# Kernel optimization log

Measured on AMD Instinct MI355X. Metric: run time of the kernel, lower is better.

The kernel has to match this reference:

```python
import jax, jax.numpy as jnp
import numpy as np
import math

SL, BS, D, NH, PF, STRIDE, LAYERS = 2048, 4, 512, 8, 3, 1, 1
DH = D // NH
N_SPF = 9  # 0-2: hidden (a,t,v cross-attend to raw inputs); 3-5: cross (at,tv,va, shared for reverse dir); 6-8: self
EMBED_SCALE = math.sqrt(D)


def _ln(x, g, b):
    m = x.mean(-1, keepdims=True)
    var = ((x - m) ** 2).mean(-1, keepdims=True)
    return (x - m) / jnp.sqrt(var + 1e-5) * g + b


def _sinusoid(sl, d):
    half = d // 2
    inv = jnp.exp(jnp.arange(half, dtype=jnp.float32) * (-math.log(10000.0) / (half - 1)))
    ang = jnp.arange(sl, dtype=jnp.float32)[:, None] * inv[None, :]
    return jnp.concatenate([jnp.sin(ang), jnp.cos(ang)], axis=-1)  # (sl, d)


def setup_inputs() -> dict:
    key = jax.random.key(0)
    ks = jax.random.split(key, 16)
    s = 0.02
    p = {}
    p['a'] = jax.random.normal(ks[0], (SL, BS, D), jnp.float32)
    p['t'] = jax.random.normal(ks[1], (SL, BS, D), jnp.float32)
    p['v'] = jax.random.normal(ks[2], (SL, BS, D), jnp.float32)
    p['init_hiddens'] = s * jax.random.normal(ks[3], (3, D), jnp.float32)
    # stacked MultiheadAttention weights for the 9 SPF blocks
    p['wq'] = s * jax.random.normal(ks[4], (N_SPF, D, D), jnp.float32)
    p['bq'] = jnp.zeros((N_SPF, D), jnp.float32)
    p['wk'] = s * jax.random.normal(ks[5], (N_SPF, D, D), jnp.float32)
    p['bk'] = jnp.zeros((N_SPF, D), jnp.float32)
    p['wv'] = s * jax.random.normal(ks[6], (N_SPF, D, D), jnp.float32)
    p['bv'] = jnp.zeros((N_SPF, D), jnp.float32)
    p['wo'] = s * jax.random.normal(ks[7], (N_SPF, D, D), jnp.float32)
    p['bo'] = jnp.zeros((N_SPF, D), jnp.float32)
    p['ln_g'] = jnp.ones((N_SPF, D), jnp.float32)
    p['ln_b'] = jnp.zeros((N_SPF, D), jnp.float32)
    p['lnkv_g'] = jnp.ones((N_SPF, D), jnp.float32)
    p['lnkv_b'] = jnp.zeros((N_SPF, D), jnp.float32)
    # stacked FFN weights for the 9 FFN blocks
    p['w1'] = s * jax.random.normal(ks[8], (N_SPF, 4 * D, D), jnp.float32)
    p['b1'] = jnp.zeros((N_SPF, 4 * D), jnp.float32)
    p['w2'] = s * jax.random.normal(ks[9], (N_SPF, D, 4 * D), jnp.float32)
    p['b2'] = jnp.zeros((N_SPF, D), jnp.float32)
    p['fln_g'] = jnp.ones((N_SPF, D), jnp.float32)
    p['fln_b'] = jnp.zeros((N_SPF, D), jnp.float32)
    p['out_g'] = jnp.ones((D,), jnp.float32)
    p['out_b'] = jnp.zeros((D,), jnp.float32)
    return p


def reference(a, t, v, init_hiddens, wq, bq, wk, bk, wv, bv, wo, bo,
              ln_g, ln_b, lnkv_g, lnkv_b, w1, b1, w2, b2, fln_g, fln_b,
              out_g, out_b):
    scale = DH ** -0.5
    # precomputed strided modulo gather indices: r[i,j] = (i+1)*stride - pf + j
    idx = ((jnp.arange(SL) + 1) * STRIDE - PF)[:, None] + jnp.arange(PF)[None, :]  # (SL, PF)

    def spf(i, x, ctx, has_kv):
        # x: (SL, BS, D); ctx: (CL, BS, D) or None (self-attention on normed x)
        res = x
        xn = _ln(x, ln_g[i], ln_b[i])
        c = xn if ctx is None else ctx
        kv = c[idx % c.shape[0]]                      # (SL, PF, BS, D) modulo-gathered window
        if has_kv:
            kv = _ln(kv, lnkv_g[i], lnkv_b[i])
        q = (xn @ wq[i].T + bq[i]).reshape(SL, BS, NH, DH) * scale
        k = (kv @ wk[i].T + bk[i]).reshape(SL, PF, BS, NH, DH)
        vv = (kv @ wv[i].T + bv[i]).reshape(SL, PF, BS, NH, DH)
        attn = jax.nn.softmax(jnp.einsum('sbnd,spbnd->sbnp', q, k), axis=-1)
        o = jnp.einsum('sbnp,spbnd->sbnd', attn, vv).reshape(SL, BS, D)
        return res + o @ wo[i].T + bo[i]

    def ffn(i, x):
        h = jax.nn.relu(_ln(x, fln_g[i], fln_b[i]) @ w1[i].T + b1[i])
        return x + h @ w2[i].T + b2[i]

    pos = _sinusoid(SL, D)[:, None, :]
    a = a * EMBED_SCALE + pos
    t = t * EMBED_SCALE + pos
    v = v * EMBED_SCALE + pos
    h_a = jnp.broadcast_to(init_hiddens[0], (SL, BS, D))
    h_t = jnp.broadcast_to(init_hiddens[1], (SL, BS, D))
    h_v = jnp.broadcast_to(init_hiddens[2], (SL, BS, D))

    for _ in range(LAYERS):
        # hidden layer: hiddens cross-attend to raw modality streams
        h_a = ffn(0, spf(0, h_a, a, True))
        h_t = ffn(1, spf(1, h_t, t, True))
        h_v = ffn(2, spf(2, h_v, v, True))
        # cross layer: six branches, three shared weight sets (forward/reverse)
        h_at = ffn(3, spf(3, h_a, h_t, True))
        h_tv = ffn(4, spf(4, h_t, h_v, True))
        h_va = ffn(5, spf(5, h_v, h_a, True))
        h_ta = ffn(3, spf(3, h_t, h_a, True))
        h_vt = ffn(4, spf(4, h_v, h_t, True))
        h_av = ffn(5, spf(5, h_a, h_v, True))
        h_a, h_t, h_v = h_at + h_av, h_ta + h_tv, h_va + h_vt
        # self layer
        h_a = ffn(6, spf(6, h_a, None, False))
        h_t = ffn(7, spf(7, h_t, None, False))
        h_v = ffn(8, spf(8, h_v, None, False))

    return jnp.stack([_ln(h_a, out_g, out_b), _ln(h_t, out_g, out_b), _ln(h_v, out_g, out_b)])
```

## Files before the change

kernel.cpp:

```cpp
#include <hip/hip_runtime.h>

#define SL 2048
#define BS 4
#define DM 512
#define NH 8
#define DH 64
#define RD 8192
#define DF 2048

#define BM 128
#define BK 32

typedef unsigned short u16;
typedef __attribute__((ext_vector_type(8))) short short8;
typedef __attribute__((ext_vector_type(4))) float f32x4;

__device__ __forceinline__ float bf2f(u16 u) {
  return __uint_as_float(((unsigned)u) << 16);
}
__device__ __forceinline__ u16 f2bf(float f) {
  unsigned u = __float_as_uint(f);
  unsigned r = (u + 0x7fffu + ((u >> 16) & 1u)) >> 16;
  return (u16)r;
}

typedef __attribute__((address_space(3))) unsigned int lds_u32;
typedef __attribute__((address_space(1))) unsigned int gbl_u32;
__device__ __forceinline__ void gload_lds16(const void* g, void* l) {
  __builtin_amdgcn_global_load_lds((gbl_u32*)g, (lds_u32*)l, 16, 0, 0);
}

struct GemmDesc {
  const u16* A;
  const u16* B;
  const float* bias;
  const float* res;
  u16* Cb;
  float* Cf;
  float bmul;
  int relu;
  int accum;
};
struct GemmBatch { GemmDesc d[9]; };

struct LnDesc { const float* x; const float* g; const float* b; u16* yb; float* yf; };
struct LnBatch { LnDesc d[6]; };

struct AttnDesc { const u16* Q; const u16* K; const u16* V; u16* O; };
struct AttnBatch { AttnDesc d[3]; };

struct CvtDesc { const float* src; u16* dst; int n8; float scale; };
struct CvtBatch { CvtDesc d[6]; };

struct EmbBatch { const float* src[3]; float* dst[3]; const float* pos; };

template<int TBN>
__global__ __launch_bounds__(256) void gemm_k(GemmBatch args, int N, int K) {
  constexpr int NFR = TBN / 32;
  constexpr int BU = TBN / 64;
  GemmDesc g = args.d[blockIdx.z];
  __shared__ u16 As[2][BM * BK];
  __shared__ u16 Bs[2][TBN * BK];
  const int t = threadIdx.x;
  const int w = t >> 6, l = t & 63;
  const u16* Ag = g.A + (size_t)blockIdx.y * BM * K;
  const u16* Bg = g.B + (size_t)blockIdx.x * TBN * K;
  f32x4 acc[4][NFR];
#pragma unroll
  for (int m = 0; m < 4; ++m)
#pragma unroll
    for (int n = 0; n < NFR; ++n) acc[m][n] = f32x4{0.f, 0.f, 0.f, 0.f};
  const int wr = (w >> 1) * 64;
  const int wc = (w & 1) * (TBN / 2);
  const int lr = l & 15;
  const int cxo = ((l >> 4) ^ (l & 3)) << 3;

  auto stage = [&](int buf, int k0) {
#pragma unroll
    for (int i = 0; i < 2; ++i) {
      const int u = (i << 8) + t;
      const int row = u >> 2;
      const int c = (u & 3) ^ (row & 3);
      gload_lds16(Ag + (size_t)row * K + k0 + (c << 3),
                  (char*)&As[buf][0] + (i << 12) + (w << 10));
    }
#pragma unroll
    for (int i = 0; i < BU; ++i) {
      const int u = (i << 8) + t;
      const int row = u >> 2;
      const int c = (u & 3) ^ (row & 3);
      gload_lds16(Bg + (size_t)row * K + k0 + (c << 3),
                  (char*)&Bs[buf][0] + (i << 12) + (w << 10));
    }
  };

  stage(0, 0);
  const int nt = K / BK;
  int cur = 0;
  for (int it = 0; it < nt; ++it) {
    __syncthreads();
    if (it + 1 < nt) stage(cur ^ 1, (it + 1) * BK);
    const u16* Ab = &As[cur][0];
    const u16* Bb = &Bs[cur][0];
    short8 af[4], bfr[NFR];
#pragma unroll
    for (int m = 0; m < 4; ++m)
      af[m] = *(const short8*)(Ab + (wr + m * 16 + lr) * BK + cxo);
#pragma unroll
    for (int n = 0; n < NFR; ++n)
      bfr[n] = *(const short8*)(Bb + (wc + n * 16 + lr) * BK + cxo);
#pragma unroll
    for (int m = 0; m < 4; ++m)
#pragma unroll
      for (int n = 0; n < NFR; ++n)
        acc[m][n] = __builtin_amdgcn_mfma_f32_16x16x32_bf16(af[m], bfr[n], acc[m][n], 0, 0, 0);
    cur ^= 1;
  }

  const int c0 = blockIdx.x * TBN + wc + lr;
  const int r0 = blockIdx.y * BM + wr + ((l >> 4) << 2);
#pragma unroll
  for (int n = 0; n < NFR; ++n) {
    const int gc = c0 + n * 16;
    const float bi = g.bias ? g.bias[gc] * g.bmul : 0.f;
#pragma unroll
    for (int m = 0; m < 4; ++m) {
#pragma unroll
      for (int r = 0; r < 4; ++r) {
        const size_t off = (size_t)(r0 + m * 16 + r) * N + gc;
        float v = acc[m][n][r] + bi;
        if (g.res) v += g.res[off];
        if (g.relu) v = fmaxf(v, 0.f);
        if (g.Cb) {
          g.Cb[off] = f2bf(v);
        } else {
          if (g.accum) v += g.Cf[off];
          g.Cf[off] = v;
        }
      }
    }
  }
}

__global__ __launch_bounds__(256) void ln_k(LnBatch args) {
  LnDesc d = args.d[blockIdx.y];
  const int row = blockIdx.x * 4 + (threadIdx.x >> 6);
  const int l = threadIdx.x & 63;
  const float* xp = d.x + (size_t)row * DM + l * 8;
  float4 x0 = *(const float4*)xp;
  float4 x1 = *(const float4*)(xp + 4);
  float xv[8] = {x0.x, x0.y, x0.z, x0.w, x1.x, x1.y, x1.z, x1.w};
  float s = 0.f, ss = 0.f;
#pragma unroll
  for (int j = 0; j < 8; ++j) { s += xv[j]; ss += xv[j] * xv[j]; }
#pragma unroll
  for (int m = 1; m < 64; m <<= 1) {
    s += __shfl_xor(s, m, 64);
    ss += __shfl_xor(ss, m, 64);
  }
  const float mean = s * (1.f / DM);
  const float var = ss * (1.f / DM) - mean * mean;
  const float rstd = rsqrtf(var + 1e-5f);
  float4 g0 = *(const float4*)(d.g + l * 8);
  float4 g1 = *(const float4*)(d.g + l * 8 + 4);
  float4 b0 = *(const float4*)(d.b + l * 8);
  float4 b1 = *(const float4*)(d.b + l * 8 + 4);
  float gv[8] = {g0.x, g0.y, g0.z, g0.w, g1.x, g1.y, g1.z, g1.w};
  float bv[8] = {b0.x, b0.y, b0.z, b0.w, b1.x, b1.y, b1.z, b1.w};
  float y[8];
#pragma unroll
  for (int j = 0; j < 8; ++j) y[j] = (xv[j] - mean) * rstd * gv[j] + bv[j];
  if (d.yb) {
    short8 p;
#pragma unroll
    for (int j = 0; j < 8; ++j) p[j] = (short)f2bf(y[j]);
    *(short8*)(d.yb + (size_t)row * DM + l * 8) = p;
  } else {
    float* o = d.yf + (size_t)row * DM + l * 8;
    *(float4*)o = float4{y[0], y[1], y[2], y[3]};
    *(float4*)(o + 4) = float4{y[4], y[5], y[6], y[7]};
  }
}

__global__ __launch_bounds__(256) void attn_k(AttnBatch args) {
  AttnDesc d = args.d[blockIdx.y];
  const int idx = blockIdx.x * 256 + threadIdx.x;
  const int h = idx & 7;
  const int b = (idx >> 3) & 3;
  const int s = idx >> 5;
  const int s0 = (s + SL - 2) & (SL - 1);
  const int s1 = (s + SL - 1) & (SL - 1);
  const size_t rq = (size_t)(s * BS + b) * DM + h * DH;
  const size_t r0 = (size_t)(s0 * BS + b) * DM + h * DH;
  const size_t r1 = (size_t)(s1 * BS + b) * DM + h * DH;
  float d0 = 0.f, d1 = 0.f, d2 = 0.f;
#pragma unroll
  for (int c = 0; c < 8; ++c) {
    short8 q8 = *(const short8*)(d.Q + rq + c * 8);
    short8 k0 = *(const short8*)(d.K + r0 + c * 8);
    short8 k1 = *(const short8*)(d.K + r1 + c * 8);
    short8 k2 = *(const short8*)(d.K + rq + c * 8);
#pragma unroll
    for (int e = 0; e < 8; ++e) {
      const float q = bf2f((u16)q8[e]);
      d0 += q * bf2f((u16)k0[e]);
      d1 += q * bf2f((u16)k1[e]);
      d2 += q * bf2f((u16)k2[e]);
    }
  }
  const float mx = fmaxf(d0, fmaxf(d1, d2));
  float e0 = expf(d0 - mx), e1 = expf(d1 - mx), e2 = expf(d2 - mx);
  const float inv = 1.f / (e0 + e1 + e2);
  e0 *= inv; e1 *= inv; e2 *= inv;
#pragma unroll
  for (int c = 0; c < 8; ++c) {
    short8 v0 = *(const short8*)(d.V + r0 + c * 8);
    short8 v1 = *(const short8*)(d.V + r1 + c * 8);
    short8 v2 = *(const short8*)(d.V + rq + c * 8);
    short8 o8;
#pragma unroll
    for (int e = 0; e < 8; ++e)
      o8[e] = (short)f2bf(e0 * bf2f((u16)v0[e]) + e1 * bf2f((u16)v1[e]) + e2 * bf2f((u16)v2[e]));
    *(short8*)(d.O + rq + c * 8) = o8;
  }
}

__global__ __launch_bounds__(256) void cvt_k(CvtBatch a) {
  CvtDesc d = a.d[blockIdx.y];
  const int stride = gridDim.x * 256;
  for (int i = blockIdx.x * 256 + threadIdx.x; i < d.n8; i += stride) {
    float4 x0 = ((const float4*)d.src)[i * 2];
    float4 x1 = ((const float4*)d.src)[i * 2 + 1];
    short8 r;
    r[0] = (short)f2bf(x0.x * d.scale); r[1] = (short)f2bf(x0.y * d.scale);
    r[2] = (short)f2bf(x0.z * d.scale); r[3] = (short)f2bf(x0.w * d.scale);
    r[4] = (short)f2bf(x1.x * d.scale); r[5] = (short)f2bf(x1.y * d.scale);
    r[6] = (short)f2bf(x1.z * d.scale); r[7] = (short)f2bf(x1.w * d.scale);
    *(short8*)(d.dst + (size_t)i * 8) = r;
  }
}

__global__ __launch_bounds__(256) void pos_k(float* pos) {
  const int i = blockIdx.x * 256 + threadIdx.x;
  const int dd = i & (DM - 1);
  const int s = i >> 9;
  const int j = (dd < 256) ? dd : dd - 256;
  const float inv = expf((float)j * -0.036119374f);
  const float ang = (float)s * inv;
  pos[i] = (dd < 256) ? sinf(ang) : cosf(ang);
}

__global__ __launch_bounds__(256) void embed_k(EmbBatch a) {
  const int z = blockIdx.y;
  const int i = blockIdx.x * 256 + threadIdx.x;
  float4 x = ((const float4*)a.src[z])[i];
  const int e = i << 2;
  const int dcol = e & (DM - 1);
  const int srow = e >> 11;
  float4 p = *(const float4*)(a.pos + (size_t)srow * DM + dcol);
  const float SC = 22.627417f;
  float4 y{x.x * SC + p.x, x.y * SC + p.y, x.z * SC + p.z, x.w * SC + p.w};
  ((float4*)a.dst[z])[i] = y;
}

__global__ __launch_bounds__(256) void hinit_k(const float* init, float* H) {
  const int z = blockIdx.y;
  const int i = blockIdx.x * 256 + threadIdx.x;
  float4 w = ((const float4*)(init + z * DM))[i & 127];
  ((float4*)(H + (size_t)z * RD * DM))[i] = w;
}

extern "C" void kernel_launch(void* const* d_in, const int* in_sizes, int n_in,
                              void* d_out, int out_size, void* d_ws, size_t ws_size,
                              hipStream_t stream) {
  (void)in_sizes; (void)n_in; (void)out_size;
  const float* in_a  = (const float*)d_in[0];
  const float* in_t  = (const float*)d_in[1];
  const float* in_v  = (const float*)d_in[2];
  const float* initH = (const float*)d_in[3];
  const float* wq = (const float*)d_in[4];
  const float* bq = (const float*)d_in[5];
  const float* wk = (const float*)d_in[6];
  const float* bk = (const float*)d_in[7];
  const float* wv = (const float*)d_in[8];
  const float* bv = (const float*)d_in[9];
  const float* wo = (const float*)d_in[10];
  const float* bo = (const float*)d_in[11];
  const float* ln_g = (const float*)d_in[12];
  const float* ln_b = (const float*)d_in[13];
  const float* lnkv_g = (const float*)d_in[14];
  const float* lnkv_b = (const float*)d_in[15];
  const float* w1 = (const float*)d_in[16];
  const float* b1 = (const float*)d_in[17];
  const float* w2 = (const float*)d_in[18];
  const float* b2 = (const float*)d_in[19];
  const float* fln_g = (const float*)d_in[20];
  const float* fln_b = (const float*)d_in[21];
  const float* out_g = (const float*)d_in[22];
  const float* out_b = (const float*)d_in[23];
  float* out = (float*)d_out;

  char* ws = (char*)d_ws;
  u16* wq_b = (u16*)(ws + 0);
  u16* wk_b = (u16*)(ws + 4718592);
  u16* wv_b = (u16*)(ws + 9437184);
  u16* wo_b = (u16*)(ws + 14155776);
  u16* w1_b = (u16*)(ws + 18874368);
  u16* w2_b = (u16*)(ws + 37748736);
  const size_t slotF = (size_t)RD * DM * 4;
  const size_t slotB = (size_t)RD * DM * 2;
  const size_t oH = 56623104;
  const size_t oS = oH + 3 * slotF;
  const size_t oX = oS + 6 * slotF;
  int G = 1;
  if (ws_size >= oX + 15 * slotB) G = 3;
  else if (ws_size >= oX + 10 * slotB) G = 2;

  float* Hs[3]; float* Ss[6];
  for (int j = 0; j < 3; ++j) Hs[j] = (float*)(ws + oH + j * slotF);
  for (int i = 0; i < 6; ++i) Ss[i] = (float*)(ws + oS + i * slotF);
  auto SLOT = [&](int j) { return (u16*)(ws + oX + (size_t)j * slotB); };
  auto KN = [&](int j) { return SLOT(j); };
  auto XN = [&](int j) { return SLOT(G + j); };
  auto QS = [&](int j) { return SLOT(2 * G + 3 * j); };
  auto KS = [&](int j) { return SLOT(2 * G + 3 * j + 1); };
  auto VS = [&](int j) { return SLOT(2 * G + 3 * j + 2); };
  auto F1 = [&](int j) { return SLOT(G + 4 * j); };

  {
    CvtBatch cb{};
    cb.d[0] = CvtDesc{wq, wq_b, 294912, 0.125f};
    cb.d[1] = CvtDesc{wk, wk_b, 294912, 1.f};
    cb.d[2] = CvtDesc{wv, wv_b, 294912, 1.f};
    cb.d[3] = CvtDesc{wo, wo_b, 294912, 1.f};
    cb.d[4] = CvtDesc{w1, w1_b, 1179648, 1.f};
    cb.d[5] = CvtDesc{w2, w2_b, 1179648, 1.f};
    cvt_k<<<dim3(512, 6), 256, 0, stream>>>(cb);
  }
  float* pos = (float*)(ws + oX);
  pos_k<<<dim3(4096), 256, 0, stream>>>(pos);
  {
    EmbBatch eb{};
    eb.src[0] = in_a; eb.src[1] = in_t; eb.src[2] = in_v;
    eb.dst[0] = Ss[3]; eb.dst[1] = Ss[4]; eb.dst[2] = Ss[5];
    eb.pos = pos;
    embed_k<<<dim3(4096, 3), 256, 0, stream>>>(eb);
  }
  hinit_k<<<dim3(4096, 3), 256, 0, stream>>>(initH, (float*)(ws + oH));

  auto run_group = [&](int g, float* const* xv, float* const* ctx, const int* wi,
                       float* const* sout, float* const* fout, int accum) {
    {
      LnBatch lb{}; int nd = 0;
      for (int j = 0; j < g; ++j)
        lb.d[nd++] = LnDesc{xv[j], ln_g + wi[j] * DM, ln_b + wi[j] * DM, XN(j), nullptr};
      if (ctx)
        for (int j = 0; j < g; ++j)
          lb.d[nd++] = LnDesc{ctx[j], lnkv_g + wi[j] * DM, lnkv_b + wi[j] * DM, KN(j), nullptr};
      ln_k<<<dim3(2048, nd), 256, 0, stream>>>(lb);
    }
    {
      GemmBatch gb{}; int nd = 0;
      for (int j = 0; j < g; ++j)
        gb.d[nd++] = GemmDesc{XN(j), wq_b + (size_t)wi[j] * DM * DM, bq + wi[j] * DM,
                              nullptr, QS(j), nullptr, 0.125f, 0, 0};
      for (int j = 0; j < g; ++j)
        gb.d[nd++] = GemmDesc{ctx ? KN(j) : XN(j), wk_b + (size_t)wi[j] * DM * DM, bk + wi[j] * DM,
                              nullptr, KS(j), nullptr, 1.f, 0, 0};
      for (int j = 0; j < g; ++j)
        gb.d[nd++] = GemmDesc{ctx ? KN(j) : XN(j), wv_b + (size_t)wi[j] * DM * DM, bv + wi[j] * DM,
                              nullptr, VS(j), nullptr, 1.f, 0, 0};
      gemm_k<64><<<dim3(DM / 64, RD / BM, nd), 256, 0, stream>>>(gb, DM, DM);
    }
    {
      AttnBatch ab{};
      for (int j = 0; j < g; ++j) ab.d[j] = AttnDesc{QS(j), KS(j), VS(j), XN(j)};
      attn_k<<<dim3(256, g), 256, 0, stream>>>(ab);
    }
    {
      GemmBatch gb{};
      for (int j = 0; j < g; ++j)
        gb.d[j] = GemmDesc{XN(j), wo_b + (size_t)wi[j] * DM * DM, bo + wi[j] * DM,
                           xv[j], nullptr, sout[j], 1.f, 0, 0};
      gemm_k<64><<<dim3(DM / 64, RD / BM, g), 256, 0, stream>>>(gb, DM, DM);
    }
    {
      LnBatch lb{};
      for (int j = 0; j < g; ++j)
        lb.d[j] = LnDesc{sout[j], fln_g + wi[j] * DM, fln_b + wi[j] * DM, KN(j), nullptr};
      ln_k<<<dim3(2048, g), 256, 0, stream>>>(lb);
    }
    {
      GemmBatch gb{};
      for (int j = 0; j < g; ++j)
        gb.d[j] = GemmDesc{KN(j), w1_b + (size_t)wi[j] * DF * DM, b1 + wi[j] * DF,
                           nullptr, F1(j), nullptr, 1.f, 1, 0};
      gemm_k<128><<<dim3(DF / 128, RD / BM, g), 256, 0, stream>>>(gb, DF, DM);
    }
    {
      GemmBatch gb{};
      for (int j = 0; j < g; ++j)
        gb.d[j] = GemmDesc{F1(j), w2_b + (size_t)wi[j] * DM * DF, b2 + wi[j] * DM,
                           sout[j], nullptr, fout[j], 1.f, 0, accum};
      gemm_k<64><<<dim3(DM / 64, RD / BM, g), 256, 0, stream>>>(gb, DM, DF);
    }
  };

  auto drive = [&](int n, float* const* xv, float* const* ctx, const int* wi,
                   float* const* sout, float* const* fout, int accum) {
    for (int b = 0; b < n; b += G) {
      const int g = (G < n - b) ? G : n - b;
      run_group(g, xv + b, ctx ? ctx + b : nullptr, wi + b, sout + b, fout + b, accum);
    }
  };

  {
    float* xv[3] = {Hs[0], Hs[1], Hs[2]};
    float* ctx[3] = {Ss[3], Ss[4], Ss[5]};
    const int wi[3] = {0, 1, 2};
    float* sout[3] = {Ss[0], Ss[1], Ss[2]};
    float* fout[3] = {Hs[0], Hs[1], Hs[2]};
    drive(3, xv, ctx, wi, sout, fout, 0);
  }
  {
    float* xv[3] = {Hs[0], Hs[1], Hs[2]};
    float* ctx[3] = {Hs[1], Hs[2], Hs[0]};
    const int wi[3] = {3, 4, 5};
    float* sout[3] = {Ss[0], Ss[1], Ss[2]};
    drive(3, xv, ctx, wi, sout, sout, 0);
  }
  {
    float* xv[3] = {Hs[1], Hs[2], Hs[0]};
    float* ctx[3] = {Hs[0], Hs[1], Hs[2]};
    const int wi[3] = {3, 4, 5};
    float* sout[3] = {Ss[3], Ss[4], Ss[5]};
    float* fout[3] = {Ss[1], Ss[2], Ss[0]};
    drive(3, xv, ctx, wi, sout, fout, 1);
  }
  {
    float* xv[3] = {Ss[0], Ss[1], Ss[2]};
    const int wi[3] = {6, 7, 8};
    float* sout[3] = {Ss[3], Ss[4], Ss[5]};
    float* fout[3] = {Hs[0], Hs[1], Hs[2]};
    drive(3, xv, nullptr, wi, sout, fout, 0);
  }
  {
    LnBatch lb{};
    for (int j = 0; j < 3; ++j)
      lb.d[j] = LnDesc{Hs[j], out_g, out_b, nullptr, out + (size_t)j * RD * DM};
    ln_k<<<dim3(2048, 3), 256, 0, stream>>>(lb);
  }
}
```

Measured before the change: 2.454 ms.

## Pack QKV weights, fuse embedding into LN, swizzle GEMM grid, split FFN

Packs the Q, K and V weights into one matrix, so projections run as a single wide-N GEMM writing an interleaved 1536-column buffer that attention reads directly. The embedding scale plus positional add moves into the KV LayerNorm, which removes the separate embed kernel. The GEMM gets a workgroup-index swizzle for L2 locality and a new LDS XOR swizzle pattern. The FFN is split into two K-halves so the intermediate buffer shrinks, and the output buffer is reused as scratch, which lowers workspace needs so more branches can be grouped. In exchange the FFN does extra read-modify-write accumulation passes.

```diff
diff --git a/kernel.cpp b/kernel.cpp
--- a/kernel.cpp
+++ b/kernel.cpp
@@ -7,8 +7,6 @@
 #define DH 64
 #define RD 8192
 #define DF 2048
-
-#define BM 128
 #define BK 32
 
 typedef unsigned short u16;
@@ -37,34 +35,51 @@
   const float* res;
   u16* Cb;
   float* Cf;
-  float bmul;
+  int K;
+  int ldb;
+  int nx;
+  int ldc;
+  int col0;
   int relu;
   int accum;
 };
 struct GemmBatch { GemmDesc d[9]; };
 
-struct LnDesc { const float* x; const float* g; const float* b; u16* yb; float* yf; };
+struct LnDesc {
+  const float* x;
+  const float* raw;
+  const float* pos;
+  const float* g; const float* b;
+  u16* yb; float* yf;
+};
 struct LnBatch { LnDesc d[6]; };
 
-struct AttnDesc { const u16* Q; const u16* K; const u16* V; u16* O; };
+struct AttnDesc { const u16* PK; u16* O; };
 struct AttnBatch { AttnDesc d[3]; };
 
-struct CvtDesc { const float* src; u16* dst; int n8; float scale; };
-struct CvtBatch { CvtDesc d[6]; };
-
-struct EmbBatch { const float* src[3]; float* dst[3]; const float* pos; };
+struct CvtDesc { const float* src; u16* dst; int n8; };
+struct CvtBatch { CvtDesc d[3]; };
 
 template<int TBN>
-__global__ __launch_bounds__(256) void gemm_k(GemmBatch args, int N, int K) {
+__global__ __launch_bounds__(256) void gemm_k(GemmBatch args) {
   constexpr int NFR = TBN / 32;
   constexpr int BU = TBN / 64;
-  GemmDesc g = args.d[blockIdx.z];
-  __shared__ u16 As[2][BM * BK];
+  const GemmDesc g = args.d[blockIdx.z];
+  __shared__ u16 As[2][128 * BK];
   __shared__ u16 Bs[2][TBN * BK];
+  const int gX = gridDim.x;
+  const int nwg = gX << 6;
+  const int orig = blockIdx.y * gX + blockIdx.x;
+  const int swz = (orig & 7) * (nwg >> 3) + (orig >> 3);
+  const int by = swz / gX;
+  const int bx = swz - by * gX;
+  if (bx >= g.nx) return;
+  const int K = g.K;
+  const int ldb = g.ldb;
   const int t = threadIdx.x;
   const int w = t >> 6, l = t & 63;
-  const u16* Ag = g.A + (size_t)blockIdx.y * BM * K;
-  const u16* Bg = g.B + (size_t)blockIdx.x * TBN * K;
+  const u16* Ag = g.A + (size_t)by * 128 * K;
+  const u16* Bg = g.B + (size_t)bx * TBN * ldb;
   f32x4 acc[4][NFR];
 #pragma unroll
   for (int m = 0; m < 4; ++m)
@@ -73,14 +88,14 @@
   const int wr = (w >> 1) * 64;
   const int wc = (w & 1) * (TBN / 2);
   const int lr = l & 15;
-  const int cxo = ((l >> 4) ^ (l & 3)) << 3;
+  const int cxo = ((l >> 4) ^ ((l >> 1) & 3)) << 3;
 
   auto stage = [&](int buf, int k0) {
 #pragma unroll
     for (int i = 0; i < 2; ++i) {
       const int u = (i << 8) + t;
       const int row = u >> 2;
-      const int c = (u & 3) ^ (row & 3);
+      const int c = (u & 3) ^ ((row >> 1) & 3);
       gload_lds16(Ag + (size_t)row * K + k0 + (c << 3),
                   (char*)&As[buf][0] + (i << 12) + (w << 10));
     }
@@ -88,8 +103,8 @@
     for (int i = 0; i < BU; ++i) {
       const int u = (i << 8) + t;
       const int row = u >> 2;
-      const int c = (u & 3) ^ (row & 3);
-      gload_lds16(Bg + (size_t)row * K + k0 + (c << 3),
+      const int c = (u & 3) ^ ((row >> 1) & 3);
+      gload_lds16(Bg + (size_t)row * ldb + k0 + (c << 3),
                   (char*)&Bs[buf][0] + (i << 12) + (w << 10));
     }
   };
@@ -117,17 +132,17 @@
     cur ^= 1;
   }
 
-  const int c0 = blockIdx.x * TBN + wc + lr;
-  const int r0 = blockIdx.y * BM + wr + ((l >> 4) << 2);
+  const int c0 = bx * TBN + wc + lr;
+  const int r0 = by * 128 + wr + ((l >> 4) << 2);
 #pragma unroll
   for (int n = 0; n < NFR; ++n) {
     const int gc = c0 + n * 16;
-    const float bi = g.bias ? g.bias[gc] * g.bmul : 0.f;
+    const float bi = g.bias ? g.bias[gc] : 0.f;
 #pragma unroll
     for (int m = 0; m < 4; ++m) {
 #pragma unroll
       for (int r = 0; r < 4; ++r) {
-        const size_t off = (size_t)(r0 + m * 16 + r) * N + gc;
+        const size_t off = (size_t)(r0 + m * 16 + r) * g.ldc + g.col0 + gc;
         float v = acc[m][n][r] + bi;
         if (g.res) v += g.res[off];
         if (g.relu) v = fmaxf(v, 0.f);
@@ -146,10 +161,23 @@
   LnDesc d = args.d[blockIdx.y];
   const int row = blockIdx.x * 4 + (threadIdx.x >> 6);
   const int l = threadIdx.x & 63;
-  const float* xp = d.x + (size_t)row * DM + l * 8;
-  float4 x0 = *(const float4*)xp;
-  float4 x1 = *(const float4*)(xp + 4);
-  float xv[8] = {x0.x, x0.y, x0.z, x0.w, x1.x, x1.y, x1.z, x1.w};
+  float xv[8];
+  if (d.raw) {
+    const float* rp = d.raw + (size_t)row * DM + l * 8;
+    const float* pp = d.pos + (size_t)(row >> 2) * DM + l * 8;
+    float4 r0 = *(const float4*)rp, r1 = *(const float4*)(rp + 4);
+    float4 p0 = *(const float4*)pp, p1 = *(const float4*)(pp + 4);
+    const float SC = 22.627416998f;
+    xv[0] = r0.x * SC + p0.x; xv[1] = r0.y * SC + p0.y;
+    xv[2] = r0.z * SC + p0.z; xv[3] = r0.w * SC + p0.w;
+    xv[4] = r1.x * SC + p1.x; xv[5] = r1.y * SC + p1.y;
+    xv[6] = r1.z * SC + p1.z; xv[7] = r1.w * SC + p1.w;
+  } else {
+    const float* xp = d.x + (size_t)row * DM + l * 8;
+    float4 x0 = *(const float4*)xp, x1 = *(const float4*)(xp + 4);
+    xv[0] = x0.x; xv[1] = x0.y; xv[2] = x0.z; xv[3] = x0.w;
+    xv[4] = x1.x; xv[5] = x1.y; xv[6] = x1.z; xv[7] = x1.w;
+  }
   float s = 0.f, ss = 0.f;
 #pragma unroll
   for (int j = 0; j < 8; ++j) { s += xv[j]; ss += xv[j] * xv[j]; }
@@ -190,16 +218,16 @@
   const int s = idx >> 5;
   const int s0 = (s + SL - 2) & (SL - 1);
   const int s1 = (s + SL - 1) & (SL - 1);
-  const size_t rq = (size_t)(s * BS + b) * DM + h * DH;
-  const size_t r0 = (size_t)(s0 * BS + b) * DM + h * DH;
-  const size_t r1 = (size_t)(s1 * BS + b) * DM + h * DH;
+  const size_t bq_ = (size_t)(s * BS + b) * 1536 + h * DH;
+  const size_t b0 = (size_t)(s0 * BS + b) * 1536 + h * DH;
+  const size_t b1 = (size_t)(s1 * BS + b) * 1536 + h * DH;
   float d0 = 0.f, d1 = 0.f, d2 = 0.f;
 #pragma unroll
   for (int c = 0; c < 8; ++c) {
-    short8 q8 = *(const short8*)(d.Q + rq + c * 8);
-    short8 k0 = *(const short8*)(d.K + r0 + c * 8);
-    short8 k1 = *(const short8*)(d.K + r1 + c * 8);
-    short8 k2 = *(const short8*)(d.K + rq + c * 8);
+    short8 q8 = *(const short8*)(d.PK + bq_ + c * 8);
+    short8 k0 = *(const short8*)(d.PK + b0 + 512 + c * 8);
+    short8 k1 = *(const short8*)(d.PK + b1 + 512 + c * 8);
+    short8 k2 = *(const short8*)(d.PK + bq_ + 512 + c * 8);
 #pragma unroll
     for (int e = 0; e < 8; ++e) {
       const float q = bf2f((u16)q8[e]);
@@ -212,17 +240,47 @@
   float e0 = expf(d0 - mx), e1 = expf(d1 - mx), e2 = expf(d2 - mx);
   const float inv = 1.f / (e0 + e1 + e2);
   e0 *= inv; e1 *= inv; e2 *= inv;
+  const size_t ro = (size_t)(s * BS + b) * DM + h * DH;
 #pragma unroll
   for (int c = 0; c < 8; ++c) {
-    short8 v0 = *(const short8*)(d.V + r0 + c * 8);
-    short8 v1 = *(const short8*)(d.V + r1 + c * 8);
-    short8 v2 = *(const short8*)(d.V + rq + c * 8);
+    short8 v0 = *(const short8*)(d.PK + b0 + 1024 + c * 8);
+    short8 v1 = *(const short8*)(d.PK + b1 + 1024 + c * 8);
+    short8 v2 = *(const short8*)(d.PK + bq_ + 1024 + c * 8);
     short8 o8;
 #pragma unroll
     for (int e = 0; e < 8; ++e)
       o8[e] = (short)f2bf(e0 * bf2f((u16)v0[e]) + e1 * bf2f((u16)v1[e]) + e2 * bf2f((u16)v2[e]));
-    *(short8*)(d.O + rq + c * 8) = o8;
-  }
+    *(short8*)(d.O + ro + c * 8) = o8;
+  }
+}
+
+__global__ __launch_bounds__(256) void packqkv_k(const float* wq, const float* wk,
+                                                 const float* wv, u16* dst) {
+  const int i = blockIdx.x * 256 + threadIdx.x;
+  const int br = i / 98304;
+  const int r = i - br * 98304;
+  const int sec = r / 32768;
+  const int r2 = r - sec * 32768;
+  const float* src = (sec == 0) ? wq : (sec == 1) ? wk : wv;
+  const float* sp = src + (size_t)br * 262144 + (size_t)r2 * 8;
+  const float sc = (sec == 0) ? 0.125f : 1.f;
+  short8 o;
+#pragma unroll
+  for (int e = 0; e < 8; ++e) o[e] = (short)f2bf(sp[e] * sc);
+  *(short8*)(dst + (size_t)br * 786432 + (size_t)sec * 262144 + (size_t)r2 * 8) = o;
+}
+
+__global__ __launch_bounds__(256) void packbias_k(const float* bq, const float* bk,
+                                                  const float* bv, float* dst) {
+  const int i = blockIdx.x * 256 + threadIdx.x;
+  if (i >= 13824) return;
+  const int br = i / 1536;
+  const int r = i - br * 1536;
+  const int sec = r >> 9;
+  const int j = r & 511;
+  float v = (sec == 0) ? bq[br * 512 + j] * 0.125f
+          : (sec == 1) ? bk[br * 512 + j] : bv[br * 512 + j];
+  dst[i] = v;
 }
 
 __global__ __launch_bounds__(256) void cvt_k(CvtBatch a) {
@@ -232,10 +290,10 @@
     float4 x0 = ((const float4*)d.src)[i * 2];
     float4 x1 = ((const float4*)d.src)[i * 2 + 1];
     short8 r;
-    r[0] = (short)f2bf(x0.x * d.scale); r[1] = (short)f2bf(x0.y * d.scale);
-    r[2] = (short)f2bf(x0.z * d.scale); r[3] = (short)f2bf(x0.w * d.scale);
-    r[4] = (short)f2bf(x1.x * d.scale); r[5] = (short)f2bf(x1.y * d.scale);
-    r[6] = (short)f2bf(x1.z * d.scale); r[7] = (short)f2bf(x1.w * d.scale);
+    r[0] = (short)f2bf(x0.x); r[1] = (short)f2bf(x0.y);
+    r[2] = (short)f2bf(x0.z); r[3] = (short)f2bf(x0.w);
+    r[4] = (short)f2bf(x1.x); r[5] = (short)f2bf(x1.y);
+    r[6] = (short)f2bf(x1.z); r[7] = (short)f2bf(x1.w);
     *(short8*)(d.dst + (size_t)i * 8) = r;
   }
 }
@@ -248,19 +306,6 @@
   const float inv = expf((float)j * -0.036119374f);
   const float ang = (float)s * inv;
   pos[i] = (dd < 256) ? sinf(ang) : cosf(ang);
-}
-
-__global__ __launch_bounds__(256) void embed_k(EmbBatch a) {
-  const int z = blockIdx.y;
-  const int i = blockIdx.x * 256 + threadIdx.x;
-  float4 x = ((const float4*)a.src[z])[i];
-  const int e = i << 2;
-  const int dcol = e & (DM - 1);
-  const int srow = e >> 11;
-  float4 p = *(const float4*)(a.pos + (size_t)srow * DM + dcol);
-  const float SC = 22.627417f;
-  float4 y{x.x * SC + p.x, x.y * SC + p.y, x.z * SC + p.z, x.w * SC + p.w};
-  ((float4*)a.dst[z])[i] = y;
 }
 
 __global__ __launch_bounds__(256) void hinit_k(const float* init, float* H) {
@@ -301,153 +346,156 @@
   float* out = (float*)d_out;
 
   char* ws = (char*)d_ws;
-  u16* wq_b = (u16*)(ws + 0);
-  u16* wk_b = (u16*)(ws + 4718592);
-  u16* wv_b = (u16*)(ws + 9437184);
-  u16* wo_b = (u16*)(ws + 14155776);
-  u16* w1_b = (u16*)(ws + 18874368);
-  u16* w2_b = (u16*)(ws + 37748736);
   const size_t slotF = (size_t)RD * DM * 4;
   const size_t slotB = (size_t)RD * DM * 2;
-  const size_t oH = 56623104;
-  const size_t oS = oH + 3 * slotF;
-  const size_t oX = oS + 6 * slotF;
+  u16* wqkv_b = (u16*)(ws);
+  u16* wo_b   = (u16*)(ws + 14155776);
+  u16* w1_b   = (u16*)(ws + 18874368);
+  u16* w2_b   = (u16*)(ws + 37748736);
+  float* bqkv = (float*)(ws + 56623104);
+  const size_t oH = 56678400;
+  float* Hs[3];  float* Acc[3];
+  for (int j = 0; j < 3; ++j) Hs[j]  = (float*)(ws + oH + (size_t)j * slotF);
+  for (int j = 0; j < 3; ++j) Acc[j] = out + (size_t)j * RD * DM;
+  float* pos = (float*)(ws + oH + 3 * slotF);
+  const size_t oL = oH + 3 * slotF + 4194304;
+  const size_t laneSz = 5 * slotB;
   int G = 1;
-  if (ws_size >= oX + 15 * slotB) G = 3;
-  else if (ws_size >= oX + 10 * slotB) G = 2;
-
-  float* Hs[3]; float* Ss[6];
-  for (int j = 0; j < 3; ++j) Hs[j] = (float*)(ws + oH + j * slotF);
-  for (int i = 0; i < 6; ++i) Ss[i] = (float*)(ws + oS + i * slotF);
-  auto SLOT = [&](int j) { return (u16*)(ws + oX + (size_t)j * slotB); };
-  auto KN = [&](int j) { return SLOT(j); };
-  auto XN = [&](int j) { return SLOT(G + j); };
-  auto QS = [&](int j) { return SLOT(2 * G + 3 * j); };
-  auto KS = [&](int j) { return SLOT(2 * G + 3 * j + 1); };
-  auto VS = [&](int j) { return SLOT(2 * G + 3 * j + 2); };
-  auto F1 = [&](int j) { return SLOT(G + 4 * j); };
-
+  if (ws_size >= oL + 3 * laneSz) G = 3;
+  else if (ws_size >= oL + 2 * laneSz) G = 2;
+
+  auto PSLOT = [&](int j, int k) {
+    return (u16*)(ws + oL + (size_t)j * laneSz + (size_t)k * slotB);
+  };
+  auto SOUT = [&](int j) { return (float*)PSLOT(j, 0); };
+
+  packqkv_k<<<dim3(3456), 256, 0, stream>>>(wq, wk, wv, wqkv_b);
+  packbias_k<<<dim3(54), 256, 0, stream>>>(bq, bk, bv, bqkv);
   {
     CvtBatch cb{};
-    cb.d[0] = CvtDesc{wq, wq_b, 294912, 0.125f};
-    cb.d[1] = CvtDesc{wk, wk_b, 294912, 1.f};
-    cb.d[2] = CvtDesc{wv, wv_b, 294912, 1.f};
-    cb.d[3] = CvtDesc{wo, wo_b, 294912, 1.f};
-    cb.d[4] = CvtDesc{w1, w1_b, 1179648, 1.f};
-    cb.d[5] = CvtDesc{w2, w2_b, 1179648, 1.f};
-    cvt_k<<<dim3(512, 6), 256, 0, stream>>>(cb);
-  }
-  float* pos = (float*)(ws + oX);
+    cb.d[0] = CvtDesc{wo, wo_b, 294912};
+    cb.d[1] = CvtDesc{w1, w1_b, 1179648};
+    cb.d[2] = CvtDesc{w2, w2_b, 1179648};
+    cvt_k<<<dim3(1024, 3), 256, 0, stream>>>(cb);
+  }
   pos_k<<<dim3(4096), 256, 0, stream>>>(pos);
-  {
-    EmbBatch eb{};
-    eb.src[0] = in_a; eb.src[1] = in_t; eb.src[2] = in_v;
-    eb.dst[0] = Ss[3]; eb.dst[1] = Ss[4]; eb.dst[2] = Ss[5];
-    eb.pos = pos;
-    embed_k<<<dim3(4096, 3), 256, 0, stream>>>(eb);
-  }
   hinit_k<<<dim3(4096, 3), 256, 0, stream>>>(initH, (float*)(ws + oH));
 
-  auto run_group = [&](int g, float* const* xv, float* const* ctx, const int* wi,
-                       float* const* sout, float* const* fout, int accum) {
+  auto run_group = [&](int g, float* const* xv, float* const* ctx, const float* const* raw,
+                       const int* wi, float* const* fout, int accum) {
     {
       LnBatch lb{}; int nd = 0;
       for (int j = 0; j < g; ++j)
-        lb.d[nd++] = LnDesc{xv[j], ln_g + wi[j] * DM, ln_b + wi[j] * DM, XN(j), nullptr};
-      if (ctx)
+        lb.d[nd++] = LnDesc{xv[j], nullptr, nullptr,
+                            ln_g + wi[j] * DM, ln_b + wi[j] * DM, PSLOT(j, 3), nullptr};
+      if (ctx || raw)
         for (int j = 0; j < g; ++j)
-          lb.d[nd++] = LnDesc{ctx[j], lnkv_g + wi[j] * DM, lnkv_b + wi[j] * DM, KN(j), nullptr};
+          lb.d[nd++] = LnDesc{ctx ? ctx[j] : nullptr, raw ? raw[j] : nullptr, pos,
+                              lnkv_g + wi[j] * DM, lnkv_b + wi[j] * DM, PSLOT(j, 4), nullptr};
       ln_k<<<dim3(2048, nd), 256, 0, stream>>>(lb);
     }
     {
-      GemmBatch gb{}; int nd = 0;
-      for (int j = 0; j < g; ++j)
-        gb.d[nd++] = GemmDesc{XN(j), wq_b + (size_t)wi[j] * DM * DM, bq + wi[j] * DM,
-                              nullptr, QS(j), nullptr, 0.125f, 0, 0};
-      for (int j = 0; j < g; ++j)
-        gb.d[nd++] = GemmDesc{ctx ? KN(j) : XN(j), wk_b + (size_t)wi[j] * DM * DM, bk + wi[j] * DM,
-                              nullptr, KS(j), nullptr, 1.f, 0, 0};
-      for (int j = 0; j < g; ++j)
-        gb.d[nd++] = GemmDesc{ctx ? KN(j) : XN(j), wv_b + (size_t)wi[j] * DM * DM, bv + wi[j] * DM,
-                              nullptr, VS(j), nullptr, 1.f, 0, 0};
-      gemm_k<64><<<dim3(DM / 64, RD / BM, nd), 256, 0, stream>>>(gb, DM, DM);
+      GemmBatch gb{}; int nz = 0, gx;
+      if (!ctx && !raw) {
+        for (int j = 0; j < g; ++j)
+          gb.d[nz++] = GemmDesc{PSLOT(j, 3), wqkv_b + (size_t)wi[j] * 786432,
+                                bqkv + wi[j] * 1536, nullptr, PSLOT(j, 0), nullptr,
+                                512, 512, 12, 1536, 0, 0, 0};
+        gx = 12;
+      } else {
+        for (int j = 0; j < g; ++j) {
+          gb.d[nz++] = GemmDesc{PSLOT(j, 3), wqkv_b + (size_t)wi[j] * 786432,
+                                bqkv + wi[j] * 1536, nullptr, PSLOT(j, 0), nullptr,
+                                512, 512, 4, 1536, 0, 0, 0};
+          gb.d[nz++] = GemmDesc{PSLOT(j, 4), wqkv_b + (size_t)wi[j] * 786432 + 262144,
+                                bqkv + wi[j] * 1536 + 512, nullptr, PSLOT(j, 0), nullptr,
+                                512, 512, 8, 1536, 512, 0, 0};
+        }
+        gx = 8;
+      }
+      gemm_k<128><<<dim3(gx, 64, nz), 256, 0, stream>>>(gb);
     }
     {
       AttnBatch ab{};
-      for (int j = 0; j < g; ++j) ab.d[j] = AttnDesc{QS(j), KS(j), VS(j), XN(j)};
+      for (int j = 0; j < g; ++j) ab.d[j] = AttnDesc{PSLOT(j, 0), PSLOT(j, 3)};
       attn_k<<<dim3(256, g), 256, 0, stream>>>(ab);
     }
     {
       GemmBatch gb{};
       for (int j = 0; j < g; ++j)
-        gb.d[j] = GemmDesc{XN(j), wo_b + (size_t)wi[j] * DM * DM, bo + wi[j] * DM,
-                           xv[j], nullptr, sout[j], 1.f, 0, 0};
-      gemm_k<64><<<dim3(DM / 64, RD / BM, g), 256, 0, stream>>>(gb, DM, DM);
+        gb.d[j] = GemmDesc{PSLOT(j, 3), wo_b + (size_t)wi[j] * DM * DM, bo + wi[j] * DM,
+                           xv[j], nullptr, SOUT(j), 512, 512, 8, 512, 0, 0, 0};
+      gemm_k<64><<<dim3(8, 64, g), 256, 0, stream>>>(gb);
     }
     {
       LnBatch lb{};
       for (int j = 0; j < g; ++j)
-        lb.d[j] = LnDesc{sout[j], fln_g + wi[j] * DM, fln_b + wi[j] * DM, KN(j), nullptr};
+        lb.d[j] = LnDesc{SOUT(j), nullptr, nullptr,
+                         fln_g + wi[j] * DM, fln_b + wi[j] * DM, PSLOT(j, 4), nullptr};
       ln_k<<<dim3(2048, g), 256, 0, stream>>>(lb);
     }
-    {
-      GemmBatch gb{};
-      for (int j = 0; j < g; ++j)
-        gb.d[j] = GemmDesc{KN(j), w1_b + (size_t)wi[j] * DF * DM, b1 + wi[j] * DF,
-                           nullptr, F1(j), nullptr, 1.f, 1, 0};
-      gemm_k<128><<<dim3(DF / 128, RD / BM, g), 256, 0, stream>>>(gb, DF, DM);
-    }
-    {
-      GemmBatch gb{};
-      for (int j = 0; j < g; ++j)
-        gb.d[j] = GemmDesc{F1(j), w2_b + (size_t)wi[j] * DM * DF, b2 + wi[j] * DM,
-                           sout[j], nullptr, fout[j], 1.f, 0, accum};
-      gemm_k<64><<<dim3(DM / 64, RD / BM, g), 256, 0, stream>>>(gb, DM, DF);
+    for (int h = 0; h < 2; ++h) {
+      {
+        GemmBatch gb{};
+        for (int j = 0; j < g; ++j)
+          gb.d[j] = GemmDesc{PSLOT(j, 4), w1_b + (size_t)wi[j] * DF * DM + (size_t)h * 524288,
+                             b1 + wi[j] * DF + h * 1024, nullptr, PSLOT(j, 2), nullptr,
+                             512, 512, 8, 1024, 0, 1, 0};
+        gemm_k<128><<<dim3(8, 64, g), 256, 0, stream>>>(gb);
+      }
+      {
+        GemmBatch gb{};
+        for (int j = 0; j < g; ++j)
+          gb.d[j] = GemmDesc{PSLOT(j, 2), w2_b + (size_t)wi[j] * DM * DF + (size_t)h * 1024,
+                             h == 0 ? b2 + wi[j] * DM : nullptr,
+                             h == 0 ? SOUT(j) : nullptr, nullptr, fout[j],
+                             1024, 2048, 8, 512, 0, 0, h == 0 ? accum : 1};
+        gemm_k<64><<<dim3(8, 64, g), 256, 0, stream>>>(gb);
+      }
     }
   };
 
-  auto drive = [&](int n, float* const* xv, float* const* ctx, const int* wi,
-                   float* const* sout, float* const* fout, int accum) {
+  auto drive = [&](int n, float* const* xv, float* const* ctx, const float* const* raw,
+                   const int* wi, float* const* fout, int accum) {
     for (int b = 0; b < n; b += G) {
       const int g = (G < n - b) ? G : n - b;
-      run_group(g, xv + b, ctx ? ctx + b : nullptr, wi + b, sout + b, fout + b, accum);
+      run_group(g, xv + b, ctx ? ctx + b : nullptr, raw ? raw + b : nullptr,
+                wi + b, fout + b, accum);
     }
   };
 
   {
     float* xv[3] = {Hs[0], Hs[1], Hs[2]};
-    float* ctx[3] = {Ss[3], Ss[4], Ss[5]};
+    const float* raw[3] = {in_a, in_t, in_v};
     const int wi[3] = {0, 1, 2};
-    float* sout[3] = {Ss[0], Ss[1], Ss[2]};
     float* fout[3] = {Hs[0], Hs[1], Hs[2]};
-    drive(3, xv, ctx, wi, sout, fout, 0);
+    drive(3, xv, nullptr, raw, wi, fout, 0);
   }
   {
     float* xv[3] = {Hs[0], Hs[1], Hs[2]};
     float* ctx[3] = {Hs[1], Hs[2], Hs[0]};
     const int wi[3] = {3, 4, 5};
-    float* sout[3] = {Ss[0], Ss[1], Ss[2]};
-    drive(3, xv, ctx, wi, sout, sout, 0);
+    float* fout[3] = {Acc[0], Acc[1], Acc[2]};
+    drive(3, xv, ctx, nullptr, wi, fout, 0);
   }
   {
     float* xv[3] = {Hs[1], Hs[2], Hs[0]};
     float* ctx[3] = {Hs[0], Hs[1], Hs[2]};
     const int wi[3] = {3, 4, 5};
-    float* sout[3] = {Ss[3], Ss[4], Ss[5]};
-    float* fout[3] = {Ss[1], Ss[2], Ss[0]};
-    drive(3, xv, ctx, wi, sout, fout, 1);
+    float* fout[3] = {Acc[1], Acc[2], Acc[0]};
+    drive(3, xv, ctx, nullptr, wi, fout, 1);
   }
   {
-    float* xv[3] = {Ss[0], Ss[1], Ss[2]};
+    float* xv[3] = {Acc[0], Acc[1], Acc[2]};
     const int wi[3] = {6, 7, 8};
-    float* sout[3] = {Ss[3], Ss[4], Ss[5]};
     float* fout[3] = {Hs[0], Hs[1], Hs[2]};
-    drive(3, xv, nullptr, wi, sout, fout, 0);
+    drive(3, xv, nullptr, nullptr, wi, fout, 0);
   }
   {
     LnBatch lb{};
     for (int j = 0; j < 3; ++j)
-      lb.d[j] = LnDesc{Hs[j], out_g, out_b, nullptr, out + (size_t)j * RD * DM};
+      lb.d[j] = LnDesc{Hs[j], nullptr, nullptr, out_g, out_b, nullptr,
+                       out + (size_t)j * RD * DM};
     ln_k<<<dim3(2048, 3), 256, 0, stream>>>(lb);
   }
 }
```

After: 2.246 ms. 1.09x faster.
